# Performance work log

Hardware: AMD Instinct MI355X
Metric: run time of the kernel (lower is better)

## Reference

```python
import jax, jax.numpy as jnp
import numpy as np

WORLD_SIZE = 4  # number of simulated ring ranks


def setup_inputs() -> dict:
    key = jax.random.key(0)
    k1, k2, k3 = jax.random.split(key, 3)
    B, S, H, D = 1, 4096, 8, 64
    q = jax.random.normal(k1, (B, S, H, D), dtype=jnp.float32)
    k = jax.random.normal(k2, (B, S, H, D), dtype=jnp.float32)
    v = jax.random.normal(k3, (B, S, H, D), dtype=jnp.float32)
    return {"q": q, "k": k, "v": v}


def reference(q, k, v):
    """Zigzag ring flash attention (causal). The ring steps with online
    sigmoid/logsigmoid LSE merging compute *exact* global causal softmax
    attention; each rank's local output is the zigzag-gathered slice of the
    global result. We compute global causal attention once, then gather the
    per-rank zigzag chunks, returning (out, lse) stacked over ranks.
    out: [W, B, S/W, H, D]; lse: [W, B, H, S/W] (flash-attn lse layout)."""
    B, S, H, D = q.shape
    W = WORLD_SIZE
    scale = 1.0 / jnp.sqrt(jnp.asarray(D, dtype=q.dtype))  # default softmax_scale

    scores = jnp.einsum('bshd,bthd->bhst', q, k) * scale  # [B,H,S,S]
    causal = jnp.tril(jnp.ones((S, S), dtype=bool))
    scores = jnp.where(causal, scores, -jnp.inf)
    lse = jax.nn.logsumexp(scores, axis=-1)               # [B,H,S]
    p = jnp.exp(scores - lse[..., None])                  # [B,H,S,S]
    out = jnp.einsum('bhst,bthd->bshd', p, v)             # [B,S,H,D]

    # zigzag chunk assignment: rank r owns global chunks [r, 2W-1-r]
    C = S // (2 * W)
    idx = jnp.array([[r, 2 * W - 1 - r] for r in range(W)])  # [W,2]

    out_c = out.reshape(B, 2 * W, C, H, D)[:, idx]        # [B,W,2,C,H,D]
    out_zig = jnp.transpose(out_c, (1, 0, 2, 3, 4, 5)).reshape(W, B, 2 * C, H, D)

    lse_c = lse.reshape(B, H, 2 * W, C)[:, :, idx]        # [B,H,W,2,C]
    lse_zig = jnp.transpose(lse_c, (2, 0, 1, 3, 4)).reshape(W, B, H, 2 * C)

    return out_zig.astype(q.dtype), lse_zig
```

## Files before the change

### kernel.cpp

```cpp
#include <hip/hip_runtime.h>
#include <hip/hip_bf16.h>
#include <math.h>
#include <stdint.h>

#define S_LEN 4096
#define NH 8
#define HD 64
#define NKT 64
#define MAXC 4

typedef __attribute__((ext_vector_type(8))) short bf16x8;
typedef __attribute__((ext_vector_type(4))) short short4v;
typedef __attribute__((ext_vector_type(4))) float f32x4;

__device__ __forceinline__ short f2bf(float f) {
    union { float f; unsigned u; } v; v.f = f;
    unsigned r = (v.u + 0x7fffu + ((v.u >> 16) & 1u)) >> 16;
    return (short)r;
}
__device__ __forceinline__ float bf2f(unsigned short u) {
    union { unsigned u; float f; } v; v.u = ((unsigned)u) << 16;
    return v.f;
}

#if __has_builtin(__builtin_amdgcn_mfma_f32_16x16x16bf16_1k)
__device__ __forceinline__ f32x4 mfma16(short4v a, short4v b, f32x4 c) {
    return __builtin_amdgcn_mfma_f32_16x16x16bf16_1k(a, b, c, 0, 0, 0);
}
#elif __has_builtin(__builtin_amdgcn_mfma_f32_16x16x16_bf16)
__device__ __forceinline__ f32x4 mfma16(short4v a, short4v b, f32x4 c) {
    return __builtin_amdgcn_mfma_f32_16x16x16_bf16(a, b, c, 0, 0, 0);
}
#else
__device__ __forceinline__ f32x4 mfma16(short4v a, short4v b, f32x4 c) {
    bf16x8 a8 = {a[0],a[1],a[2],a[3],0,0,0,0};
    bf16x8 b8 = {b[0],b[1],b[2],b[3],0,0,0,0};
    return __builtin_amdgcn_mfma_f32_16x16x32_bf16(a8, b8, c, 0, 0, 0);
}
#endif

__device__ __forceinline__ void gll16(const void* g, void* l) {
#if __has_builtin(__builtin_amdgcn_global_load_lds)
    __builtin_amdgcn_global_load_lds(
        (const __attribute__((address_space(1))) unsigned int*)(uintptr_t)g,
        (__attribute__((address_space(3))) unsigned int*)(unsigned int)(uintptr_t)l,
        16, 0, 0);
#else
    *(bf16x8*)l = *(const bf16x8*)g;
#endif
}

__global__ __launch_bounds__(256)
void zz_prep(const float* __restrict__ K, const float* __restrict__ V,
             short* __restrict__ Kbf, short* __restrict__ Vtbf) {
    const int h = blockIdx.x & 7, kt = blockIdx.x >> 3;
    const int tid = threadIdx.x;
    const int r = tid >> 2, c0 = (tid & 3) * 16;
    __shared__ short Vl[64][72];

    const float* kp = K + ((size_t)(kt * 64 + r) * NH + h) * HD + c0;
    const float* vp = V + ((size_t)(kt * 64 + r) * NH + h) * HD + c0;
    bf16x8 kv0, kv1;
    #pragma unroll
    for (int i = 0; i < 8; i += 4) {
        float4 x = *(const float4*)(kp + i);
        kv0[i+0] = f2bf(x.x); kv0[i+1] = f2bf(x.y); kv0[i+2] = f2bf(x.z); kv0[i+3] = f2bf(x.w);
        float4 x2 = *(const float4*)(kp + 8 + i);
        kv1[i+0] = f2bf(x2.x); kv1[i+1] = f2bf(x2.y); kv1[i+2] = f2bf(x2.z); kv1[i+3] = f2bf(x2.w);
        float4 y = *(const float4*)(vp + i);
        Vl[r][c0+i+0] = f2bf(y.x); Vl[r][c0+i+1] = f2bf(y.y);
        Vl[r][c0+i+2] = f2bf(y.z); Vl[r][c0+i+3] = f2bf(y.w);
        float4 y2 = *(const float4*)(vp + 8 + i);
        Vl[r][c0+8+i+0] = f2bf(y2.x); Vl[r][c0+8+i+1] = f2bf(y2.y);
        Vl[r][c0+8+i+2] = f2bf(y2.z); Vl[r][c0+8+i+3] = f2bf(y2.w);
    }
    short* kout = Kbf + ((size_t)(h * NKT + kt) * 64 + r) * 64 + c0;
    *(bf16x8*)kout = kv0;
    *(bf16x8*)(kout + 8) = kv1;
    __syncthreads();
    bf16x8 tv0, tv1;
    #pragma unroll
    for (int i = 0; i < 8; ++i) { tv0[i] = Vl[c0 + i][r]; tv1[i] = Vl[c0 + 8 + i][r]; }
    short* vout = Vtbf + ((size_t)(h * NKT + kt) * 64 + r) * 64 + c0;
    *(bf16x8*)vout = tv0;
    *(bf16x8*)(vout + 8) = tv1;
}

__global__ __launch_bounds__(256, 3)
void zz_fa_split(const float* __restrict__ Q, const short* __restrict__ Kbf,
                 const short* __restrict__ Vtbf, unsigned short* __restrict__ Po,
                 float* __restrict__ Ml) {
    const int h = blockIdx.x & 7;
    const int t = 159 - (blockIdx.x >> 3);
    int qt, c;
    if (t < 16)      { qt = t;               c = 0; }
    else if (t < 48) { qt = 16 + (t-16)/2;   c = (t-16)%2; }
    else if (t < 96) { qt = 32 + (t-48)/3;   c = (t-48)%3; }
    else             { qt = 48 + (t-96)/4;   c = (t-96)%4; }
    const int k0 = c * 16;
    const int k1 = min(k0 + 16, qt + 1);
    const int qbase = qt * 64;

    const int tid  = threadIdx.x;
    const int wave = tid >> 6;
    const int lane = tid & 63;
    const int l15  = lane & 15;
    const int quad = lane >> 4;

    __shared__ __align__(16) char smem[37888];
    short* Kb  = (short*)smem;
    short* Vt  = (short*)(smem + 8192);
    float* ObA = (float*)smem;
    float* ObB = (float*)(smem + 16896);
    float* Lb  = (float*)(smem + 33792);

    bf16x8 qf[4][2];
    #pragma unroll
    for (int nt = 0; nt < 4; ++nt) {
        #pragma unroll
        for (int kc = 0; kc < 2; ++kc) {
            const float* qp = Q + ((size_t)(qbase + nt*16 + l15) * NH + h) * HD + kc*32 + quad*8;
            float4 a = *(const float4*)qp;
            float4 b = *(const float4*)(qp + 4);
            bf16x8 f;
            f[0]=f2bf(a.x*0.125f); f[1]=f2bf(a.y*0.125f); f[2]=f2bf(a.z*0.125f); f[3]=f2bf(a.w*0.125f);
            f[4]=f2bf(b.x*0.125f); f[5]=f2bf(b.y*0.125f); f[6]=f2bf(b.z*0.125f); f[7]=f2bf(b.w*0.125f);
            qf[nt][kc] = f;
        }
    }

    f32x4 o[4][4];
    #pragma unroll
    for (int dt = 0; dt < 4; ++dt)
        #pragma unroll
        for (int nt = 0; nt < 4; ++nt) o[dt][nt] = (f32x4)0.f;
    float lloc[4] = {0.f, 0.f, 0.f, 0.f};

    const short* Ktiles = Kbf  + (size_t)h * NKT * 4096;
    const short* Vtiles = Vtbf + (size_t)h * NKT * 4096;

    for (int kt = k0; kt < k1; ++kt) {
        __syncthreads();
        const char* kg = (const char*)(Ktiles + (size_t)kt * 4096);
        const char* vg = (const char*)(Vtiles + (size_t)kt * 4096);
        #pragma unroll
        for (int i = 0; i < 2; ++i) {
            const int lo = i*4096 + tid*16;
            const int row = lo >> 7, blk = ((lo >> 4) & 7) ^ (row & 7);
            gll16(kg + row*128 + blk*16, (char*)Kb + lo);
        }
        #pragma unroll
        for (int i = 0; i < 2; ++i) {
            const int lo = i*4096 + tid*16;
            const int row = lo >> 7, blk = ((lo >> 4) & 7) ^ (row & 7);
            gll16(vg + row*128 + blk*16, (char*)Vt + lo);
        }
        __syncthreads();

        bf16x8 kf[2];
        #pragma unroll
        for (int kc = 0; kc < 2; ++kc) {
            const int row = wave*16 + l15;
            const int blk = (kc*4 + quad) ^ (l15 & 7);
            kf[kc] = *(const bf16x8*)&Kb[row*64 + blk*8];
        }

        short4v pfr[4];
        #pragma unroll
        for (int nt = 0; nt < 4; ++nt) {
            f32x4 acc = (f32x4)0.f;
            acc = __builtin_amdgcn_mfma_f32_16x16x32_bf16(kf[0], qf[nt][0], acc, 0, 0, 0);
            acc = __builtin_amdgcn_mfma_f32_16x16x32_bf16(kf[1], qf[nt][1], acc, 0, 0, 0);
            short4v pf;
            if (kt == qt) {
                #pragma unroll
                for (int r = 0; r < 4; ++r) {
                    const int key  = kt*64 + wave*16 + quad*4 + r;
                    const int qrow = qbase + nt*16 + l15;
                    const float p = (key <= qrow) ? __expf(acc[r]) : 0.f;
                    lloc[nt] += p;
                    pf[r] = f2bf(p);
                }
            } else {
                #pragma unroll
                for (int r = 0; r < 4; ++r) {
                    const float p = __expf(acc[r]);
                    lloc[nt] += p;
                    pf[r] = f2bf(p);
                }
            }
            pfr[nt] = pf;
        }

        #pragma unroll
        for (int dt = 0; dt < 4; ++dt) {
            const int row = dt*16 + l15;
            const int blk = (wave*2 + (quad >> 1)) ^ (l15 & 7);
            short4v vf = *(const short4v*)&Vt[row*64 + blk*8 + (quad & 1)*4];
            #pragma unroll
            for (int nt = 0; nt < 4; ++nt)
                o[dt][nt] = mfma16(vf, pfr[nt], o[dt][nt]);
        }
    }

    __syncthreads();
    #pragma unroll
    for (int nt = 0; nt < 4; ++nt)
        Lb[(wave*4 + quad)*64 + nt*16 + l15] = lloc[nt];
    if (wave == 1 || wave == 3) {
        float* Ob = (wave == 1) ? ObA : ObB;
        #pragma unroll
        for (int dt = 0; dt < 4; ++dt)
            #pragma unroll
            for (int nt = 0; nt < 4; ++nt)
                #pragma unroll
                for (int r = 0; r < 4; ++r)
                    Ob[(dt*16 + quad*4 + r)*66 + nt*16 + l15] = o[dt][nt][r];
    }
    __syncthreads();
    float Lfin = 0.f;
    if (wave == 0) {
        #pragma unroll
        for (int i = 0; i < 16; ++i) Lfin += Lb[i*64 + lane];
        #pragma unroll
        for (int dt = 0; dt < 4; ++dt)
            #pragma unroll
            for (int nt = 0; nt < 4; ++nt)
                #pragma unroll
                for (int r = 0; r < 4; ++r)
                    o[dt][nt][r] += ObA[(dt*16 + quad*4 + r)*66 + nt*16 + l15];
    }
    if (wave == 2) {
        #pragma unroll
        for (int dt = 0; dt < 4; ++dt)
            #pragma unroll
            for (int nt = 0; nt < 4; ++nt)
                #pragma unroll
                for (int r = 0; r < 4; ++r)
                    o[dt][nt][r] += ObB[(dt*16 + quad*4 + r)*66 + nt*16 + l15];
    }
    __syncthreads();
    if (wave == 2) {
        #pragma unroll
        for (int dt = 0; dt < 4; ++dt)
            #pragma unroll
            for (int nt = 0; nt < 4; ++nt)
                #pragma unroll
                for (int r = 0; r < 4; ++r)
                    ObA[(dt*16 + quad*4 + r)*66 + nt*16 + l15] = o[dt][nt][r];
    }
    __syncthreads();
    if (wave == 0) {
        const size_t base = (size_t)(h*MAXC + c) * S_LEN;
        #pragma unroll
        for (int dt = 0; dt < 4; ++dt) {
            #pragma unroll
            for (int nt = 0; nt < 4; ++nt) {
                short4v pk;
                #pragma unroll
                for (int r = 0; r < 4; ++r) {
                    const float v = o[dt][nt][r] + ObA[(dt*16 + quad*4 + r)*66 + nt*16 + l15];
                    pk[r] = f2bf(v);
                }
                *(short4v*)&Po[(base + qbase + nt*16 + l15)*64 + dt*16 + quad*4] = pk;
            }
        }
        Ml[base + qbase + lane] = Lfin;
    }
}

__global__ __launch_bounds__(256)
void zz_merge(const unsigned short* __restrict__ Po, const float* __restrict__ Ml,
              float* __restrict__ Out) {
    const int idx  = blockIdx.x * 256 + threadIdx.x;
    const int d    = idx & 63;
    const int qrow = (idx >> 6) & 4095;
    const int h    = idx >> 18;
    const int nc   = (qrow >> 10) + 1;

    float L = 0.f, O = 0.f;
    #pragma unroll 4
    for (int c = 0; c < nc; ++c) {
        const size_t b = (size_t)(h*MAXC + c) * S_LEN + qrow;
        L += Ml[b];
        O += bf2f(Po[b*64 + d]);
    }
    const int g    = qrow >> 9;
    const int rank = (g < 4) ? g : (7 - g);
    const int pos  = ((g < 4) ? 0 : 512) + (qrow & 511);
    Out[((size_t)(rank*1024 + pos)*NH + h)*HD + d] = O / L;
    if (d == 0)
        Out[2097152 + (rank*8 + h)*1024 + pos] = __logf(L);
}

#define QT 64
#define KT 64
#define LDP 72
__global__ __launch_bounds__(256, 4)
void zz_fa_mono(const float* __restrict__ Q, const float* __restrict__ K,
                const float* __restrict__ V, float* __restrict__ Out) {
    const int h  = blockIdx.x & 7;
    const int qt = 63 - (blockIdx.x >> 3);
    const int qbase = qt * QT;
    const int tid  = threadIdx.x;
    const int wave = tid >> 6;
    const int lane = tid & 63;
    const int l15  = lane & 15;
    const int quad = lane >> 4;

    __shared__ short Kb[KT][LDP];
    __shared__ short Vt[HD][LDP];
    __shared__ short Pb[4][16][LDP];

    const int qrow = qbase + wave * 16 + l15;
    bf16x8 qf[2];
    {
        const float* qp = Q + ((size_t)qrow * NH + h) * HD + quad * 8;
        #pragma unroll
        for (int cc = 0; cc < 2; ++cc) {
            const float* p = qp + cc * 32;
            float4 a = *(const float4*)p;
            float4 b = *(const float4*)(p + 4);
            bf16x8 f;
            f[0]=f2bf(a.x); f[1]=f2bf(a.y); f[2]=f2bf(a.z); f[3]=f2bf(a.w);
            f[4]=f2bf(b.x); f[5]=f2bf(b.y); f[6]=f2bf(b.z); f[7]=f2bf(b.w);
            qf[cc] = f;
        }
    }
    f32x4 o[4];
    #pragma unroll
    for (int nt = 0; nt < 4; ++nt) o[nt] = (f32x4)0.f;
    float m_i[4] = {-INFINITY, -INFINITY, -INFINITY, -INFINITY};
    float l_i[4] = {0.f, 0.f, 0.f, 0.f};
    const int kkK = tid >> 2, dK = (tid & 3) * 16;
    const int kkV = tid & 63, dV = (tid >> 6) * 16;
    const float scale = 0.125f;

    for (int kt = 0; kt <= qt; ++kt) {
        const int kbase = kt * KT;
        __syncthreads();
        {
            const float* kp = K + ((size_t)(kbase + kkK) * NH + h) * HD + dK;
            #pragma unroll
            for (int i = 0; i < 4; ++i) {
                float4 x = *(const float4*)(kp + i * 4);
                short4v s4;
                s4[0]=f2bf(x.x); s4[1]=f2bf(x.y); s4[2]=f2bf(x.z); s4[3]=f2bf(x.w);
                *(short4v*)&Kb[kkK][dK + i * 4] = s4;
            }
        }
        {
            const float* vp = V + ((size_t)(kbase + kkV) * NH + h) * HD + dV;
            #pragma unroll
            for (int i = 0; i < 4; ++i) {
                float4 x = *(const float4*)(vp + i * 4);
                Vt[dV + i*4 + 0][kkV] = f2bf(x.x);
                Vt[dV + i*4 + 1][kkV] = f2bf(x.y);
                Vt[dV + i*4 + 2][kkV] = f2bf(x.z);
                Vt[dV + i*4 + 3][kkV] = f2bf(x.w);
            }
        }
        __syncthreads();
        f32x4 s[4];
        #pragma unroll
        for (int nt = 0; nt < 4; ++nt) {
            f32x4 acc = (f32x4)0.f;
            #pragma unroll
            for (int kc = 0; kc < 2; ++kc) {
                bf16x8 bf = *(const bf16x8*)&Kb[nt*16 + l15][kc*32 + quad*8];
                acc = __builtin_amdgcn_mfma_f32_16x16x32_bf16(qf[kc], bf, acc, 0, 0, 0);
            }
            s[nt] = acc;
        }
        if (kt == qt) {
            #pragma unroll
            for (int nt = 0; nt < 4; ++nt) {
                const int kj = nt*16 + l15;
                #pragma unroll
                for (int r = 0; r < 4; ++r) {
                    const int qi = wave*16 + quad*4 + r;
                    s[nt][r] = (kj <= qi) ? s[nt][r] * scale : -INFINITY;
                }
            }
        } else {
            #pragma unroll
            for (int nt = 0; nt < 4; ++nt)
                #pragma unroll
                for (int r = 0; r < 4; ++r) s[nt][r] *= scale;
        }
        float alpha[4], lsum[4];
        #pragma unroll
        for (int r = 0; r < 4; ++r) {
            float mx = fmaxf(fmaxf(s[0][r], s[1][r]), fmaxf(s[2][r], s[3][r]));
            #pragma unroll
            for (int msk = 1; msk < 16; msk <<= 1)
                mx = fmaxf(mx, __shfl_xor(mx, msk));
            const float mnew = fmaxf(m_i[r], mx);
            alpha[r] = __expf(m_i[r] - mnew);
            m_i[r] = mnew;
            lsum[r] = 0.f;
        }
        #pragma unroll
        for (int nt = 0; nt < 4; ++nt) {
            #pragma unroll
            for (int r = 0; r < 4; ++r) {
                const float p = __expf(s[nt][r] - m_i[r]);
                lsum[r] += p;
                Pb[wave][quad*4 + r][nt*16 + l15] = f2bf(p);
            }
        }
        #pragma unroll
        for (int r = 0; r < 4; ++r) {
            float ls = lsum[r];
            #pragma unroll
            for (int msk = 1; msk < 16; msk <<= 1)
                ls += __shfl_xor(ls, msk);
            l_i[r] = l_i[r] * alpha[r] + ls;
        }
        #pragma unroll
        for (int nt = 0; nt < 4; ++nt)
            #pragma unroll
            for (int r = 0; r < 4; ++r)
                o[nt][r] *= alpha[r];
        bf16x8 pf[2];
        #pragma unroll
        for (int kc = 0; kc < 2; ++kc)
            pf[kc] = *(const bf16x8*)&Pb[wave][l15][kc*32 + quad*8];
        #pragma unroll
        for (int nt = 0; nt < 4; ++nt) {
            #pragma unroll
            for (int kc = 0; kc < 2; ++kc) {
                bf16x8 vf = *(const bf16x8*)&Vt[nt*16 + l15][kc*32 + quad*8];
                o[nt] = __builtin_amdgcn_mfma_f32_16x16x32_bf16(pf[kc], vf, o[nt], 0, 0, 0);
            }
        }
    }
    #pragma unroll
    for (int r = 0; r < 4; ++r) {
        const int qi   = qbase + wave*16 + quad*4 + r;
        const int g    = qi >> 9;
        const int rank = (g < 4) ? g : (7 - g);
        const int pos  = ((g < 4) ? 0 : 512) + (qi & 511);
        const float inv = 1.f / l_i[r];
        float* ob = Out + ((size_t)(rank * 1024 + pos) * NH + h) * HD;
        #pragma unroll
        for (int nt = 0; nt < 4; ++nt)
            ob[nt*16 + l15] = o[nt][r] * inv;
        if (l15 == 0)
            Out[2097152 + (rank*8 + h)*1024 + pos] = m_i[r] + __logf(l_i[r]);
    }
}

extern "C" void kernel_launch(void* const* d_in, const int* in_sizes, int n_in,
                              void* d_out, int out_size, void* d_ws, size_t ws_size,
                              hipStream_t stream) {
    const float* q = (const float*)d_in[0];
    const float* k = (const float*)d_in[1];
    const float* v = (const float*)d_in[2];
    float* out = (float*)d_out;

    const size_t kbf_elems = (size_t)NH * NKT * 64 * 64;
    const size_t po_elems  = (size_t)NH * MAXC * S_LEN * HD;
    const size_t ml_elems  = (size_t)NH * MAXC * S_LEN;
    const size_t need = kbf_elems*2*2 + po_elems*2 + ml_elems*4;

    if (ws_size >= need) {
        short* Kbf = (short*)d_ws;
        short* Vtbf = Kbf + kbf_elems;
        unsigned short* Po = (unsigned short*)(Vtbf + kbf_elems);
        float* Ml = (float*)(Po + po_elems);
        zz_prep<<<dim3(512), dim3(256), 0, stream>>>(k, v, Kbf, Vtbf);
        zz_fa_split<<<dim3(1280), dim3(256), 0, stream>>>(q, Kbf, Vtbf, Po, Ml);
        zz_merge<<<dim3((NH * S_LEN * HD) / 256), dim3(256), 0, stream>>>(Po, Ml, out);
    } else {
        zz_fa_mono<<<dim3(512), dim3(256), 0, stream>>>(q, k, v, out);
    }
}
```

Before: 131.5 us.

## Fuse split-K merge into attention kernel via last-block atomic counter

Drops the separate merge kernel. The last block to finish each query tile, found through an atomic counter that the prep kernel zeroes, sums the partial outputs and writes the final output and lse. Tiles with a single chunk write their result directly. It also balances key ranges evenly across chunks, lays waves out as a 2x2 split over queries and keys to halve per-wave accumulators, shrinks shared memory and raises occupancy to 4. In exchange it adds threadfence and atomic synchronisation, and the merge work is serialised in the last block.

```diff
diff --git a/kernel.cpp b/kernel.cpp
--- a/kernel.cpp
+++ b/kernel.cpp
@@ -50,11 +50,20 @@
 #endif
 }
 
+__device__ __forceinline__ unsigned devload_u32(const unsigned* p) {
+    return __hip_atomic_load(p, __ATOMIC_RELAXED, __HIP_MEMORY_SCOPE_AGENT);
+}
+__device__ __forceinline__ float devload_f32(const float* p) {
+    unsigned u = __hip_atomic_load((const unsigned*)p, __ATOMIC_RELAXED, __HIP_MEMORY_SCOPE_AGENT);
+    union { unsigned u; float f; } v; v.u = u; return v.f;
+}
+
 __global__ __launch_bounds__(256)
 void zz_prep(const float* __restrict__ K, const float* __restrict__ V,
-             short* __restrict__ Kbf, short* __restrict__ Vtbf) {
+             short* __restrict__ Kbf, short* __restrict__ Vtbf, int* __restrict__ Cnt) {
     const int h = blockIdx.x & 7, kt = blockIdx.x >> 3;
     const int tid = threadIdx.x;
+    if (blockIdx.x == 0) { Cnt[tid] = 0; Cnt[tid + 256] = 0; }
     const int r = tid >> 2, c0 = (tid & 3) * 16;
     __shared__ short Vl[64][72];
 
@@ -86,10 +95,11 @@
     *(bf16x8*)(vout + 8) = tv1;
 }
 
-__global__ __launch_bounds__(256, 3)
-void zz_fa_split(const float* __restrict__ Q, const short* __restrict__ Kbf,
+__global__ __launch_bounds__(256, 4)
+void zz_fa_fused(const float* __restrict__ Q, const short* __restrict__ Kbf,
                  const short* __restrict__ Vtbf, unsigned short* __restrict__ Po,
-                 float* __restrict__ Ml) {
+                 float* __restrict__ Ml, int* __restrict__ Cnt,
+                 float* __restrict__ Out) {
     const int h = blockIdx.x & 7;
     const int t = 159 - (blockIdx.x >> 3);
     int qt, c;
@@ -97,8 +107,9 @@
     else if (t < 48) { qt = 16 + (t-16)/2;   c = (t-16)%2; }
     else if (t < 96) { qt = 32 + (t-48)/3;   c = (t-48)%3; }
     else             { qt = 48 + (t-96)/4;   c = (t-96)%4; }
-    const int k0 = c * 16;
-    const int k1 = min(k0 + 16, qt + 1);
+    const int nc = (qt >> 4) + 1;
+    const int k0 = (c * (qt + 1)) / nc;
+    const int k1 = ((c + 1) * (qt + 1)) / nc;
     const int qbase = qt * 64;
 
     const int tid  = threadIdx.x;
@@ -106,20 +117,23 @@
     const int lane = tid & 63;
     const int l15  = lane & 15;
     const int quad = lane >> 4;
-
-    __shared__ __align__(16) char smem[37888];
-    short* Kb  = (short*)smem;
-    short* Vt  = (short*)(smem + 8192);
-    float* ObA = (float*)smem;
-    float* ObB = (float*)(smem + 16896);
-    float* Lb  = (float*)(smem + 33792);
-
-    bf16x8 qf[4][2];
-    #pragma unroll
-    for (int nt = 0; nt < 4; ++nt) {
+    const int kw   = wave & 1;
+    const int qw   = wave >> 1;
+
+    __shared__ __align__(16) char smem[19712];
+    short* Kb = (short*)smem;
+    short* Vt = (short*)(smem + 8192);
+    float* Tb = (float*)smem;
+    float* Lb = (float*)(smem + 17408);
+    float* Lq = (float*)(smem + 19456);
+    __shared__ int s_last;
+
+    bf16x8 qf[2][2];
+    #pragma unroll
+    for (int nt = 0; nt < 2; ++nt) {
         #pragma unroll
         for (int kc = 0; kc < 2; ++kc) {
-            const float* qp = Q + ((size_t)(qbase + nt*16 + l15) * NH + h) * HD + kc*32 + quad*8;
+            const float* qp = Q + ((size_t)(qbase + qw*32 + nt*16 + l15) * NH + h) * HD + kc*32 + quad*8;
             float4 a = *(const float4*)qp;
             float4 b = *(const float4*)(qp + 4);
             bf16x8 f;
@@ -129,12 +143,12 @@
         }
     }
 
-    f32x4 o[4][4];
+    f32x4 o[4][2];
     #pragma unroll
     for (int dt = 0; dt < 4; ++dt)
         #pragma unroll
-        for (int nt = 0; nt < 4; ++nt) o[dt][nt] = (f32x4)0.f;
-    float lloc[4] = {0.f, 0.f, 0.f, 0.f};
+        for (int nt = 0; nt < 2; ++nt) o[dt][nt] = (f32x4)0.f;
+    float lloc[2] = {0.f, 0.f};
 
     const short* Ktiles = Kbf  + (size_t)h * NKT * 4096;
     const short* Vtiles = Vtbf + (size_t)h * NKT * 4096;
@@ -157,140 +171,177 @@
         }
         __syncthreads();
 
-        bf16x8 kf[2];
-        #pragma unroll
-        for (int kc = 0; kc < 2; ++kc) {
-            const int row = wave*16 + l15;
-            const int blk = (kc*4 + quad) ^ (l15 & 7);
-            kf[kc] = *(const bf16x8*)&Kb[row*64 + blk*8];
-        }
-
-        short4v pfr[4];
-        #pragma unroll
-        for (int nt = 0; nt < 4; ++nt) {
-            f32x4 acc = (f32x4)0.f;
-            acc = __builtin_amdgcn_mfma_f32_16x16x32_bf16(kf[0], qf[nt][0], acc, 0, 0, 0);
-            acc = __builtin_amdgcn_mfma_f32_16x16x32_bf16(kf[1], qf[nt][1], acc, 0, 0, 0);
-            short4v pf;
-            if (kt == qt) {
+        bf16x8 kf[2][2];
+        #pragma unroll
+        for (int g = 0; g < 2; ++g) {
+            #pragma unroll
+            for (int kc = 0; kc < 2; ++kc) {
+                const int row = kw*32 + g*16 + l15;
+                const int blk = (kc*4 + quad) ^ (l15 & 7);
+                kf[g][kc] = *(const bf16x8*)&Kb[row*64 + blk*8];
+            }
+        }
+
+        short4v pfr[2][2];
+        const bool diag = (kt == qt);
+        #pragma unroll
+        for (int g = 0; g < 2; ++g) {
+            #pragma unroll
+            for (int nt = 0; nt < 2; ++nt) {
+                f32x4 acc = (f32x4)0.f;
+                acc = __builtin_amdgcn_mfma_f32_16x16x32_bf16(kf[g][0], qf[nt][0], acc, 0, 0, 0);
+                acc = __builtin_amdgcn_mfma_f32_16x16x32_bf16(kf[g][1], qf[nt][1], acc, 0, 0, 0);
+                short4v pf;
+                if (diag) {
+                    #pragma unroll
+                    for (int r = 0; r < 4; ++r) {
+                        const int key = kt*64 + kw*32 + g*16 + quad*4 + r;
+                        const int qr  = qbase + qw*32 + nt*16 + l15;
+                        const float p = (key <= qr) ? __expf(acc[r]) : 0.f;
+                        lloc[nt] += p;
+                        pf[r] = f2bf(p);
+                    }
+                } else {
+                    #pragma unroll
+                    for (int r = 0; r < 4; ++r) {
+                        const float p = __expf(acc[r]);
+                        lloc[nt] += p;
+                        pf[r] = f2bf(p);
+                    }
+                }
+                pfr[g][nt] = pf;
+            }
+        }
+
+        #pragma unroll
+        for (int dt = 0; dt < 4; ++dt) {
+            #pragma unroll
+            for (int g = 0; g < 2; ++g) {
+                const int row = dt*16 + l15;
+                const int blk = (kw*4 + g*2 + (quad >> 1)) ^ (l15 & 7);
+                short4v vf = *(const short4v*)&Vt[row*64 + blk*8 + (quad & 1)*4];
                 #pragma unroll
-                for (int r = 0; r < 4; ++r) {
-                    const int key  = kt*64 + wave*16 + quad*4 + r;
-                    const int qrow = qbase + nt*16 + l15;
-                    const float p = (key <= qrow) ? __expf(acc[r]) : 0.f;
-                    lloc[nt] += p;
-                    pf[r] = f2bf(p);
-                }
-            } else {
-                #pragma unroll
-                for (int r = 0; r < 4; ++r) {
-                    const float p = __expf(acc[r]);
-                    lloc[nt] += p;
-                    pf[r] = f2bf(p);
-                }
-            }
-            pfr[nt] = pf;
-        }
-
+                for (int nt = 0; nt < 2; ++nt)
+                    o[dt][nt] = mfma16(vf, pfr[g][nt], o[dt][nt]);
+            }
+        }
+    }
+
+    __syncthreads();
+    #pragma unroll
+    for (int nt = 0; nt < 2; ++nt)
+        Lb[(wave*4 + quad)*32 + nt*16 + l15] = lloc[nt];
+    if (kw == 1) {
+        #pragma unroll
+        for (int dt = 0; dt < 4; ++dt)
+            #pragma unroll
+            for (int nt = 0; nt < 2; ++nt)
+                *(f32x4*)&Tb[(qw*32 + nt*16 + l15)*68 + dt*16 + quad*4] = o[dt][nt];
+    }
+    __syncthreads();
+    if (kw == 0) {
         #pragma unroll
         for (int dt = 0; dt < 4; ++dt) {
-            const int row = dt*16 + l15;
-            const int blk = (wave*2 + (quad >> 1)) ^ (l15 & 7);
-            short4v vf = *(const short4v*)&Vt[row*64 + blk*8 + (quad & 1)*4];
-            #pragma unroll
-            for (int nt = 0; nt < 4; ++nt)
-                o[dt][nt] = mfma16(vf, pfr[nt], o[dt][nt]);
-        }
-    }
-
+            #pragma unroll
+            for (int nt = 0; nt < 2; ++nt) {
+                float* p = &Tb[(qw*32 + nt*16 + l15)*68 + dt*16 + quad*4];
+                f32x4 x = *(f32x4*)p;
+                o[dt][nt] += x;
+                *(f32x4*)p = o[dt][nt];
+            }
+        }
+    }
+    if (tid < 64) {
+        const int qw2 = tid >> 5, qi = tid & 31;
+        float L = 0.f;
+        #pragma unroll
+        for (int kw2 = 0; kw2 < 2; ++kw2)
+            #pragma unroll
+            for (int qd = 0; qd < 4; ++qd)
+                L += Lb[((qw2*2 + kw2)*4 + qd)*32 + qi];
+        Lq[tid] = L;
+    }
     __syncthreads();
-    #pragma unroll
-    for (int nt = 0; nt < 4; ++nt)
-        Lb[(wave*4 + quad)*64 + nt*16 + l15] = lloc[nt];
-    if (wave == 1 || wave == 3) {
-        float* Ob = (wave == 1) ? ObA : ObB;
-        #pragma unroll
-        for (int dt = 0; dt < 4; ++dt)
-            #pragma unroll
-            for (int nt = 0; nt < 4; ++nt)
-                #pragma unroll
-                for (int r = 0; r < 4; ++r)
-                    Ob[(dt*16 + quad*4 + r)*66 + nt*16 + l15] = o[dt][nt][r];
-    }
+
+    const int q    = tid >> 2;
+    const int ds0  = (tid & 3) * 16;
+    const int qrow = qbase + q;
+
+    if (nc == 1) {
+        const float inv = 1.f / Lq[q];
+        const int g2   = qrow >> 9;
+        const int rank = (g2 < 4) ? g2 : (7 - g2);
+        const int pos  = ((g2 < 4) ? 0 : 512) + (qrow & 511);
+        float* op = Out + ((size_t)(rank*1024 + pos)*NH + h)*HD + ds0;
+        #pragma unroll
+        for (int i = 0; i < 16; i += 4) {
+            f32x4 x = *(f32x4*)&Tb[q*68 + ds0 + i];
+            op[i+0] = x[0]*inv; op[i+1] = x[1]*inv; op[i+2] = x[2]*inv; op[i+3] = x[3]*inv;
+        }
+        if (tid < 64) {
+            const int qr2  = qbase + tid;
+            const int g3   = qr2 >> 9;
+            const int rank3 = (g3 < 4) ? g3 : (7 - g3);
+            const int pos3  = ((g3 < 4) ? 0 : 512) + (qr2 & 511);
+            Out[2097152 + (rank3*8 + h)*1024 + pos3] = __logf(Lq[tid]);
+        }
+        return;
+    }
+
+    const size_t bown = (size_t)(h*MAXC + c) * S_LEN;
+    {
+        bf16x8 a, b;
+        #pragma unroll
+        for (int i = 0; i < 8; ++i) {
+            a[i] = f2bf(Tb[q*68 + ds0 + i]);
+            b[i] = f2bf(Tb[q*68 + ds0 + 8 + i]);
+        }
+        *(bf16x8*)&Po[(bown + qrow)*64 + ds0]     = a;
+        *(bf16x8*)&Po[(bown + qrow)*64 + ds0 + 8] = b;
+    }
+    if (tid < 64) Ml[bown + qbase + tid] = Lq[tid];
+    __threadfence();
     __syncthreads();
-    float Lfin = 0.f;
-    if (wave == 0) {
-        #pragma unroll
-        for (int i = 0; i < 16; ++i) Lfin += Lb[i*64 + lane];
-        #pragma unroll
-        for (int dt = 0; dt < 4; ++dt)
-            #pragma unroll
-            for (int nt = 0; nt < 4; ++nt)
-                #pragma unroll
-                for (int r = 0; r < 4; ++r)
-                    o[dt][nt][r] += ObA[(dt*16 + quad*4 + r)*66 + nt*16 + l15];
-    }
-    if (wave == 2) {
-        #pragma unroll
-        for (int dt = 0; dt < 4; ++dt)
-            #pragma unroll
-            for (int nt = 0; nt < 4; ++nt)
-                #pragma unroll
-                for (int r = 0; r < 4; ++r)
-                    o[dt][nt][r] += ObB[(dt*16 + quad*4 + r)*66 + nt*16 + l15];
+    if (tid == 0) {
+        const int old = atomicAdd(&Cnt[h*64 + qt], 1);
+        s_last = (old == nc - 1);
     }
     __syncthreads();
-    if (wave == 2) {
-        #pragma unroll
-        for (int dt = 0; dt < 4; ++dt)
-            #pragma unroll
-            for (int nt = 0; nt < 4; ++nt)
-                #pragma unroll
-                for (int r = 0; r < 4; ++r)
-                    ObA[(dt*16 + quad*4 + r)*66 + nt*16 + l15] = o[dt][nt][r];
-    }
-    __syncthreads();
-    if (wave == 0) {
-        const size_t base = (size_t)(h*MAXC + c) * S_LEN;
-        #pragma unroll
-        for (int dt = 0; dt < 4; ++dt) {
-            #pragma unroll
-            for (int nt = 0; nt < 4; ++nt) {
-                short4v pk;
-                #pragma unroll
-                for (int r = 0; r < 4; ++r) {
-                    const float v = o[dt][nt][r] + ObA[(dt*16 + quad*4 + r)*66 + nt*16 + l15];
-                    pk[r] = f2bf(v);
-                }
-                *(short4v*)&Po[(base + qbase + nt*16 + l15)*64 + dt*16 + quad*4] = pk;
-            }
-        }
-        Ml[base + qbase + lane] = Lfin;
-    }
-}
-
-__global__ __launch_bounds__(256)
-void zz_merge(const unsigned short* __restrict__ Po, const float* __restrict__ Ml,
-              float* __restrict__ Out) {
-    const int idx  = blockIdx.x * 256 + threadIdx.x;
-    const int d    = idx & 63;
-    const int qrow = (idx >> 6) & 4095;
-    const int h    = idx >> 18;
-    const int nc   = (qrow >> 10) + 1;
-
-    float L = 0.f, O = 0.f;
-    #pragma unroll 4
-    for (int c = 0; c < nc; ++c) {
-        const size_t b = (size_t)(h*MAXC + c) * S_LEN + qrow;
-        L += Ml[b];
-        O += bf2f(Po[b*64 + d]);
-    }
-    const int g    = qrow >> 9;
-    const int rank = (g < 4) ? g : (7 - g);
-    const int pos  = ((g < 4) ? 0 : 512) + (qrow & 511);
-    Out[((size_t)(rank*1024 + pos)*NH + h)*HD + d] = O / L;
-    if (d == 0)
-        Out[2097152 + (rank*8 + h)*1024 + pos] = __logf(L);
+    if (!s_last) return;
+    __threadfence();
+
+    float acc[16];
+    #pragma unroll
+    for (int i = 0; i < 16; ++i) acc[i] = 0.f;
+    float L = 0.f;
+    for (int cc = 0; cc < nc; ++cc) {
+        const size_t bc = (size_t)(h*MAXC + cc) * S_LEN;
+        const unsigned* sp = (const unsigned*)(Po + (bc + qrow)*64 + ds0);
+        #pragma unroll
+        for (int i = 0; i < 8; ++i) {
+            const unsigned u = devload_u32(sp + i);
+            acc[2*i + 0] += bf2f((unsigned short)(u & 0xffffu));
+            acc[2*i + 1] += bf2f((unsigned short)(u >> 16));
+        }
+        L += devload_f32(&Ml[bc + qrow]);
+    }
+    const float inv = 1.f / L;
+    const int g2   = qrow >> 9;
+    const int rank = (g2 < 4) ? g2 : (7 - g2);
+    const int pos  = ((g2 < 4) ? 0 : 512) + (qrow & 511);
+    float* op = Out + ((size_t)(rank*1024 + pos)*NH + h)*HD + ds0;
+    #pragma unroll
+    for (int i = 0; i < 16; ++i) op[i] = acc[i] * inv;
+    if (tid < 64) {
+        const int qr2 = qbase + tid;
+        float L2 = 0.f;
+        for (int cc = 0; cc < nc; ++cc)
+            L2 += devload_f32(&Ml[(size_t)(h*MAXC + cc)*S_LEN + qr2]);
+        const int g3    = qr2 >> 9;
+        const int rank3 = (g3 < 4) ? g3 : (7 - g3);
+        const int pos3  = ((g3 < 4) ? 0 : 512) + (qr2 & 511);
+        Out[2097152 + (rank3*8 + h)*1024 + pos3] = __logf(L2);
+    }
 }
 
 #define QT 64
@@ -462,16 +513,16 @@
     const size_t kbf_elems = (size_t)NH * NKT * 64 * 64;
     const size_t po_elems  = (size_t)NH * MAXC * S_LEN * HD;
     const size_t ml_elems  = (size_t)NH * MAXC * S_LEN;
-    const size_t need = kbf_elems*2*2 + po_elems*2 + ml_elems*4;
+    const size_t need = kbf_elems*2*2 + po_elems*2 + ml_elems*4 + 512*4;
 
     if (ws_size >= need) {
-        short* Kbf = (short*)d_ws;
+        short* Kbf  = (short*)d_ws;
         short* Vtbf = Kbf + kbf_elems;
         unsigned short* Po = (unsigned short*)(Vtbf + kbf_elems);
         float* Ml = (float*)(Po + po_elems);
-        zz_prep<<<dim3(512), dim3(256), 0, stream>>>(k, v, Kbf, Vtbf);
-        zz_fa_split<<<dim3(1280), dim3(256), 0, stream>>>(q, Kbf, Vtbf, Po, Ml);
-        zz_merge<<<dim3((NH * S_LEN * HD) / 256), dim3(256), 0, stream>>>(Po, Ml, out);
+        int* Cnt  = (int*)(Ml + ml_elems);
+        zz_prep<<<dim3(512), dim3(256), 0, stream>>>(k, v, Kbf, Vtbf, Cnt);
+        zz_fa_fused<<<dim3(1280), dim3(256), 0, stream>>>(q, Kbf, Vtbf, Po, Ml, Cnt, out);
     } else {
         zz_fa_mono<<<dim3(512), dim3(256), 0, stream>>>(q, k, v, out);
     }
```

Measured after the change: 301.0 us. 2.29x slower.
